# Optimization experiments

Measured on AMD Instinct MI355X. Metric: run time of the kernel, lower is better.

## Reference

```python
import jax, jax.numpy as jnp
import numpy as np

B, T, IN = 4, 1024, 172
D, H, FF, L, NCLS = 512, 8, 2048, 8, 1296
HD = D // H
EPS = 1e-5


def setup_inputs() -> dict:
    key = jax.random.key(0)
    ks = jax.random.split(key, 16)
    rn = lambda k, s, sc=0.02: jax.random.normal(k, s, jnp.float32) * sc
    return {
        "poses": jax.random.normal(ks[0], (B, T, IN), jnp.float32),
        "pose_w": rn(ks[1], (D, IN)), "pose_b": jnp.zeros((D,), jnp.float32),
        "in_w": rn(ks[2], (L, 3 * D, D)), "in_b": jnp.zeros((L, 3 * D), jnp.float32),
        "out_w": rn(ks[3], (L, D, D)), "out_b": jnp.zeros((L, D), jnp.float32),
        "ln1_g": jnp.ones((L, D), jnp.float32), "ln1_b": jnp.zeros((L, D), jnp.float32),
        "ffn_w1": rn(ks[4], (L, FF, D)), "ffn_b1": jnp.zeros((L, FF), jnp.float32),
        "ffn_w2": rn(ks[5], (L, D, FF)), "ffn_b2": jnp.zeros((L, D), jnp.float32),
        "ln2_g": jnp.ones((L, D), jnp.float32), "ln2_b": jnp.zeros((L, D), jnp.float32),
        "tcn1_w": rn(ks[6], (512, D, 5)), "tcn1_b": jnp.zeros((512,), jnp.float32),
        "tcn2_w": rn(ks[7], (D, 512, 5)), "tcn2_b": jnp.zeros((D,), jnp.float32),
        "fc1_w": rn(ks[8], (128, D)), "fc1_b": jnp.zeros((128,), jnp.float32),
        "fc2_w": rn(ks[9], (NCLS, 128)), "fc2_b": jnp.zeros((NCLS,), jnp.float32),
    }


def _pos_enc(seq_len, d):
    # PositionalEncoding1D: interleaved sin/cos per frequency pair
    inv_freq = 1.0 / (10000.0 ** (jnp.arange(0, d, 2, dtype=jnp.float32) / d))
    ang = jnp.arange(seq_len, dtype=jnp.float32)[:, None] * inv_freq  # [T, d/2]
    return jnp.stack([jnp.sin(ang), jnp.cos(ang)], axis=-1).reshape(seq_len, d)


def _ln(x, g, b):
    m = x.mean(-1, keepdims=True)
    v = jnp.var(x, axis=-1, keepdims=True)
    return (x - m) * jax.lax.rsqrt(v + EPS) * g + b


def _encoder_layer(x, iw, ib, ow, ob, g1, b1, w1, c1, w2, c2, g2, b2):
    # post-norm TransformerEncoderLayer, eager (non-flash) attention
    Bc, Tc, _ = x.shape
    qkv = x @ iw.T + ib                       # [B,T,3D]
    q, k, v = jnp.split(qkv, 3, axis=-1)
    q = q.reshape(Bc, Tc, H, HD)
    k = k.reshape(Bc, Tc, H, HD)
    v = v.reshape(Bc, Tc, H, HD)
    scores = jnp.einsum('bqhd,bkhd->bhqk', q, k) / jnp.sqrt(jnp.float32(HD))
    attn = jax.nn.softmax(scores, axis=-1)    # explicit weights (need_weights=True)
    o = jnp.einsum('bhqk,bkhd->bqhd', attn, v).reshape(Bc, Tc, D)
    o = o @ ow.T + ob
    x = _ln(x + o, g1, b1)
    f = jax.nn.relu(x @ w1.T + c1) @ w2.T + c2
    return _ln(x + f, g2, b2)


def _conv1d(x, w, b):  # x [B,T,C_in], w [C_out,C_in,5], pad=2
    y = jax.lax.conv_general_dilated(
        x.transpose(0, 2, 1), w, window_strides=(1,), padding=((2, 2),),
        dimension_numbers=('NCH', 'OIH', 'NCH'))
    return y.transpose(0, 2, 1) + b


def _avgpool2(x):  # kernel=2 stride=2 along time
    Bc, Tc, C = x.shape
    return x.reshape(Bc, Tc // 2, 2, C).mean(axis=2)


def reference(poses, pose_w, pose_b, in_w, in_b, out_w, out_b, ln1_g, ln1_b,
              ffn_w1, ffn_b1, ffn_w2, ffn_b2, ln2_g, ln2_b,
              tcn1_w, tcn1_b, tcn2_w, tcn2_b, fc1_w, fc1_b, fc2_w, fc2_b):
    x = poses.reshape(poses.shape[0], poses.shape[1], -1) @ pose_w.T + pose_b
    x = x + _pos_enc(x.shape[1], D)[None]

    def run_stack(h, idx):
        for i in idx:
            h = _encoder_layer(h, in_w[i], in_b[i], out_w[i], out_b[i],
                               ln1_g[i], ln1_b[i], ffn_w1[i], ffn_b1[i],
                               ffn_w2[i], ffn_b2[i], ln2_g[i], ln2_b[i])
        return h

    h = run_stack(x, (0, 1))
    h = run_stack(h, (2, 3)) + h
    h = run_stack(h, (4, 5)) + h
    h = run_stack(h, (6, 7)) + h

    h = _avgpool2(h)                 # [B,T/2,D]
    h = _conv1d(h, tcn1_w, tcn1_b)   # [B,T/2,512]
    h = _avgpool2(h)                 # [B,T/4,512]
    h = _conv1d(h, tcn2_w, tcn2_b)   # [B,T/4,D]
    h = h @ fc1_w.T + fc1_b
    logits = h @ fc2_w.T + fc2_b     # [B,T/4,num_classes]
    return logits
```

## Files before the change

### kernel.cpp

```cpp
#include <hip/hip_runtime.h>
#include <hip/hip_bf16.h>

static constexpr int kB = 4;
static constexpr int kT = 1024;
static constexpr int kIn = 172;
static constexpr int kD = 512;
static constexpr int kH = 8;
static constexpr int kHD = 64;
static constexpr int kFF = 2048;
static constexpr int kNCLS = 1296;
static constexpr float kEps = 1e-5f;

typedef __attribute__((ext_vector_type(8))) short bf16x8_t;
typedef __attribute__((ext_vector_type(4))) float f32x4_t;
typedef __attribute__((ext_vector_type(8))) unsigned short u16x8_t;
typedef __attribute__((ext_vector_type(4))) unsigned short u16x4_t;

static __device__ __forceinline__ unsigned short f2bf(float f) {
  unsigned int u = __float_as_uint(f);
  unsigned int r = (u + 0x7fffu + ((u >> 16) & 1u)) >> 16;
  return (unsigned short)r;
}

__global__ void cvt_kernel(const float* __restrict__ src, ushort* __restrict__ dst, int n8)
{
  const int i = blockIdx.x * 256 + threadIdx.x;
  if (i >= n8) return;
  const float4 a = *(const float4*)&src[i * 8];
  const float4 b = *(const float4*)&src[i * 8 + 4];
  u16x8_t t;
  t[0] = f2bf(a.x); t[1] = f2bf(a.y); t[2] = f2bf(a.z); t[3] = f2bf(a.w);
  t[4] = f2bf(b.x); t[5] = f2bf(b.y); t[6] = f2bf(b.z); t[7] = f2bf(b.w);
  *(u16x8_t*)&dst[i * 8] = t;
}

template<int MREP, int NREP>
__global__ __launch_bounds__(256) void bgemm_kernel(
    const ushort* __restrict__ A, const ushort* __restrict__ W,
    const float* __restrict__ bias, const float* __restrict__ resid,
    float* __restrict__ C, ushort* __restrict__ Cb, int M, int N, int K, int doRelu)
{
  constexpr int BM = MREP * 32, BN = NREP * 32;
  constexpr int SRD = 72;
  constexpr int TPRA = 256 / BM, CSA = 64 / TPRA, NLA = CSA / 8;
  constexpr int TPRB = 256 / BN, CSB = 64 / TPRB, NLB = CSB / 8;
  __shared__ ushort As[BM * SRD];
  __shared__ ushort Bs[BN * SRD];

  const int tid = threadIdx.x;
  int bid = blockIdx.y * gridDim.x + blockIdx.x;
  const int nwg = gridDim.x * gridDim.y;
  if ((nwg & 7) == 0) bid = (bid & 7) * (nwg >> 3) + (bid >> 3);
  const int bm = (bid / gridDim.x) * BM, bn = (bid % gridDim.x) * BN;

  const int wv = tid >> 6, lane = tid & 63;
  const int lr = lane & 15, lg = lane >> 4;
  const int wr = wv >> 1, wc = wv & 1;

  const int ra = tid / TPRA, ca = (tid % TPRA) * CSA;
  const int rb = tid / TPRB, cb = (tid % TPRB) * CSB;

  f32x4_t acc[MREP][NREP];
#pragma unroll
  for (int mr = 0; mr < MREP; ++mr)
#pragma unroll
    for (int nr = 0; nr < NREP; ++nr) acc[mr][nr] = (f32x4_t){0.f, 0.f, 0.f, 0.f};

  u16x8_t pa[NLA], pb[NLB];
  auto loadAB = [&](int k0) {
    const ushort* ap = A + (size_t)(bm + ra) * K + k0 + ca;
#pragma unroll
    for (int j = 0; j < NLA; ++j) pa[j] = *(const u16x8_t*)(ap + j * 8);
    const ushort* bp = W + (size_t)(bn + rb) * K + k0 + cb;
#pragma unroll
    for (int j = 0; j < NLB; ++j) pb[j] = *(const u16x8_t*)(bp + j * 8);
  };
  auto storeLDS = [&]() {
#pragma unroll
    for (int j = 0; j < NLA; ++j) *(u16x8_t*)&As[ra * SRD + ca + j * 8] = pa[j];
#pragma unroll
    for (int j = 0; j < NLB; ++j) *(u16x8_t*)&Bs[rb * SRD + cb + j * 8] = pb[j];
  };

  loadAB(0);
  storeLDS();
  __syncthreads();

  const int nsteps = K >> 6;
  for (int s = 0; s < nsteps; ++s) {
    const bool more = (s + 1) < nsteps;
    if (more) loadAB((s + 1) << 6);

#pragma unroll
    for (int kk = 0; kk < 2; ++kk) {
      bf16x8_t af[MREP];
#pragma unroll
      for (int mr = 0; mr < MREP; ++mr)
        af[mr] = *(const bf16x8_t*)&As[(wr * MREP * 16 + mr * 16 + lr) * SRD + kk * 32 + lg * 8];
#pragma unroll
      for (int nr = 0; nr < NREP; ++nr) {
        const bf16x8_t bf = *(const bf16x8_t*)&Bs[(wc * NREP * 16 + nr * 16 + lr) * SRD + kk * 32 + lg * 8];
#pragma unroll
        for (int mr = 0; mr < MREP; ++mr)
          acc[mr][nr] = __builtin_amdgcn_mfma_f32_16x16x32_bf16(af[mr], bf, acc[mr][nr], 0, 0, 0);
      }
    }
    __syncthreads();
    if (more) { storeLDS(); __syncthreads(); }
  }

#pragma unroll
  for (int mr = 0; mr < MREP; ++mr) {
#pragma unroll
    for (int v = 0; v < 4; ++v) {
      const int m = bm + wr * MREP * 16 + mr * 16 + lg * 4 + v;
#pragma unroll
      for (int nr = 0; nr < NREP; ++nr) {
        const int n = bn + wc * NREP * 16 + nr * 16 + lr;
        float val = acc[mr][nr][v] + bias[n];
        if (doRelu) val = fmaxf(val, 0.f);
        if (resid) val += resid[(size_t)m * N + n];
        if (C)  C[(size_t)m * N + n] = val;
        if (Cb) Cb[(size_t)m * N + n] = f2bf(val);
      }
    }
  }
}

#define GBM 64
#define GBN 64
#define GBK 16
#define LDST 68

__global__ __launch_bounds__(256) void gemm_kernel(
    const float* __restrict__ A, const float* __restrict__ W,
    const float* __restrict__ bias, const float* __restrict__ resid,
    float* __restrict__ C, int M, int N, int K, int doRelu)
{
  __shared__ __align__(16) float As[GBK][LDST];
  __shared__ __align__(16) float Ws[GBK][LDST];
  const int tid = threadIdx.x;
  const int bm = blockIdx.y * GBM;
  const int bn = blockIdx.x * GBN;
  const int tx = tid & 15, ty = tid >> 4;
  const int li = tid >> 2;
  const int lk = (tid & 3) << 2;

  float acc[4][4];
#pragma unroll
  for (int i = 0; i < 4; ++i)
#pragma unroll
    for (int j = 0; j < 4; ++j) acc[i][j] = 0.f;

  for (int k0 = 0; k0 < K; k0 += GBK) {
    float4 av = make_float4(0.f, 0.f, 0.f, 0.f);
    float4 wv = make_float4(0.f, 0.f, 0.f, 0.f);
    {
      const int m = bm + li;
      if (m < M) {
        if (k0 + lk + 4 <= K) {
          av = *(const float4*)&A[(size_t)m * K + k0 + lk];
        } else {
          float t4[4] = {0.f, 0.f, 0.f, 0.f};
          for (int c = 0; c < 4; ++c) { int k = k0 + lk + c; if (k < K) t4[c] = A[(size_t)m * K + k]; }
          av = make_float4(t4[0], t4[1], t4[2], t4[3]);
        }
      }
      const int n = bn + li;
      if (n < N) {
        if (k0 + lk + 4 <= K) {
          wv = *(const float4*)&W[(size_t)n * K + k0 + lk];
        } else {
          float t4[4] = {0.f, 0.f, 0.f, 0.f};
          for (int c = 0; c < 4; ++c) { int k = k0 + lk + c; if (k < K) t4[c] = W[(size_t)n * K + k]; }
          wv = make_float4(t4[0], t4[1], t4[2], t4[3]);
        }
      }
    }
    __syncthreads();
    As[lk + 0][li] = av.x; As[lk + 1][li] = av.y; As[lk + 2][li] = av.z; As[lk + 3][li] = av.w;
    Ws[lk + 0][li] = wv.x; Ws[lk + 1][li] = wv.y; Ws[lk + 2][li] = wv.z; Ws[lk + 3][li] = wv.w;
    __syncthreads();
#pragma unroll
    for (int kk = 0; kk < GBK; ++kk) {
      const float4 a4 = *(const float4*)&As[kk][ty << 2];
      const float4 b4 = *(const float4*)&Ws[kk][tx << 2];
      const float a[4] = {a4.x, a4.y, a4.z, a4.w};
      const float b[4] = {b4.x, b4.y, b4.z, b4.w};
#pragma unroll
      for (int i = 0; i < 4; ++i)
#pragma unroll
        for (int j = 0; j < 4; ++j) acc[i][j] = fmaf(a[i], b[j], acc[i][j]);
    }
  }

#pragma unroll
  for (int i = 0; i < 4; ++i) {
    const int m = bm + (ty << 2) + i;
    if (m >= M) continue;
#pragma unroll
    for (int j = 0; j < 4; ++j) {
      const int n = bn + (tx << 2) + j;
      if (n >= N) continue;
      float v = acc[i][j] + bias[n];
      if (doRelu) v = fmaxf(v, 0.f);
      if (resid) v += resid[(size_t)m * N + n];
      C[(size_t)m * N + n] = v;
    }
  }
}

__global__ __launch_bounds__(256) void ln_kernel(
    float* __restrict__ X, ushort* __restrict__ Xb,
    const float* __restrict__ g, const float* __restrict__ bta,
    const float* Padd, float* Pout)
{
  const int row = blockIdx.x;
  const int tid = threadIdx.x;
  float* xr = X + (size_t)row * kD;
  const float x0 = xr[tid];
  const float x1 = xr[tid + 256];
  float s = x0 + x1;
  float q = x0 * x0 + x1 * x1;
#pragma unroll
  for (int off = 32; off > 0; off >>= 1) {
    s += __shfl_down(s, off);
    q += __shfl_down(q, off);
  }
  __shared__ float ss[4], qq[4];
  const int w = tid >> 6;
  if ((tid & 63) == 0) { ss[w] = s; qq[w] = q; }
  __syncthreads();
  const float S = ss[0] + ss[1] + ss[2] + ss[3];
  const float Q = qq[0] + qq[1] + qq[2] + qq[3];
  const float mean = S * (1.f / kD);
  const float var = Q * (1.f / kD) - mean * mean;
  const float inv = rsqrtf(var + kEps);
  float v0 = (x0 - mean) * inv * g[tid] + bta[tid];
  float v1 = (x1 - mean) * inv * g[tid + 256] + bta[tid + 256];
  if (Padd) {
    v0 += Padd[(size_t)row * kD + tid];
    v1 += Padd[(size_t)row * kD + tid + 256];
  }
  xr[tid] = v0; xr[tid + 256] = v1;
  ushort* xb = Xb + (size_t)row * kD;
  xb[tid] = f2bf(v0); xb[tid + 256] = f2bf(v1);
  if (Pout) {
    Pout[(size_t)row * kD + tid] = v0;
    Pout[(size_t)row * kD + tid + 256] = v1;
  }
}

#define KSTR 72
#define PSTR 74
__global__ __launch_bounds__(256) void attn_mfma_kernel(
    const ushort* __restrict__ qkv, ushort* __restrict__ O)
{
  const int b = blockIdx.z, h = blockIdx.y;
  const int q0 = blockIdx.x << 6;
  const int tid = threadIdx.x;
  const int wv = tid >> 6, lane = tid & 63;
  const int lr = lane & 15;
  const int lg = lane >> 4;

  __shared__ ushort Ks[64 * KSTR];
  __shared__ ushort Vt[64 * KSTR];
  __shared__ ushort Pl[4][16 * PSTR];

  bf16x8_t qa[2];
  {
    const ushort* qrow = qkv + ((size_t)(b * kT + q0 + wv * 16 + lr)) * (3 * kD) + h * kHD + lg * 8;
    qa[0] = *(const bf16x8_t*)qrow;
    qa[1] = *(const bf16x8_t*)(qrow + 32);
  }

  float m_[4], l_[4];
  f32x4_t oacc[4];
#pragma unroll
  for (int r = 0; r < 4; ++r) { m_[r] = -1e30f; l_[r] = 0.f; }
#pragma unroll
  for (int nb = 0; nb < 4; ++nb) oacc[nb] = (f32x4_t){0.f, 0.f, 0.f, 0.f};

  const int srow = tid >> 2;
  const int sd   = (tid & 3) << 4;
  const int vkp  = tid & 31;
  const int vdh  = tid >> 5;

  for (int kt = 0; kt < kT / 64; ++kt) {
    __syncthreads();
    {
      const ushort* kr = qkv + ((size_t)(b * kT + (kt << 6) + srow)) * (3 * kD) + kD + h * kHD + sd;
      *(u16x8_t*)&Ks[srow * KSTR + sd]     = *(const u16x8_t*)kr;
      *(u16x8_t*)&Ks[srow * KSTR + sd + 8] = *(const u16x8_t*)(kr + 8);
      const ushort* vr = qkv + ((size_t)(b * kT + (kt << 6) + 2 * vkp)) * (3 * kD) + 2 * kD + h * kHD + vdh * 8;
      const u16x8_t v0 = *(const u16x8_t*)vr;
      const u16x8_t v1 = *(const u16x8_t*)(vr + 3 * kD);
#pragma unroll
      for (int e = 0; e < 8; ++e) {
        const unsigned int packv = (unsigned int)v0[e] | ((unsigned int)v1[e] << 16);
        *(unsigned int*)&Vt[(vdh * 8 + e) * KSTR + 2 * vkp] = packv;
      }
    }
    __syncthreads();

    f32x4_t s[4];
#pragma unroll
    for (int cc = 0; cc < 4; ++cc) {
      const ushort* kb = &Ks[(cc * 16 + lr) * KSTR + lg * 8];
      const bf16x8_t k0 = *(const bf16x8_t*)kb;
      const bf16x8_t k1 = *(const bf16x8_t*)(kb + 32);
      f32x4_t acc = (f32x4_t){0.f, 0.f, 0.f, 0.f};
      acc = __builtin_amdgcn_mfma_f32_16x16x32_bf16(qa[0], k0, acc, 0, 0, 0);
      acc = __builtin_amdgcn_mfma_f32_16x16x32_bf16(qa[1], k1, acc, 0, 0, 0);
#pragma unroll
      for (int r = 0; r < 4; ++r) acc[r] *= 0.125f;
      s[cc] = acc;
    }

#pragma unroll
    for (int r = 0; r < 4; ++r) {
      float mx = fmaxf(fmaxf(s[0][r], s[1][r]), fmaxf(s[2][r], s[3][r]));
      mx = fmaxf(mx, __shfl_xor(mx, 1));
      mx = fmaxf(mx, __shfl_xor(mx, 2));
      mx = fmaxf(mx, __shfl_xor(mx, 4));
      mx = fmaxf(mx, __shfl_xor(mx, 8));
      const float mnew = fmaxf(m_[r], mx);
      const float alpha = __expf(m_[r] - mnew);
      float sum = 0.f;
#pragma unroll
      for (int cc = 0; cc < 4; ++cc) {
        const float p = __expf(s[cc][r] - mnew);
        s[cc][r] = p;
        sum += p;
      }
      sum += __shfl_xor(sum, 1);
      sum += __shfl_xor(sum, 2);
      sum += __shfl_xor(sum, 4);
      sum += __shfl_xor(sum, 8);
      l_[r] = l_[r] * alpha + sum;
      m_[r] = mnew;
#pragma unroll
      for (int nb = 0; nb < 4; ++nb) oacc[nb][r] *= alpha;
#pragma unroll
      for (int cc = 0; cc < 4; ++cc)
        Pl[wv][(lg * 4 + r) * PSTR + cc * 16 + lr] = f2bf(s[cc][r]);
    }

    const bf16x8_t pa0 = *(const bf16x8_t*)&Pl[wv][lr * PSTR + lg * 8];
    const bf16x8_t pa1 = *(const bf16x8_t*)&Pl[wv][lr * PSTR + 32 + lg * 8];
#pragma unroll
    for (int nb = 0; nb < 4; ++nb) {
      const ushort* vb = &Vt[(nb * 16 + lr) * KSTR + lg * 8];
      const bf16x8_t v0 = *(const bf16x8_t*)vb;
      const bf16x8_t v1 = *(const bf16x8_t*)(vb + 32);
      oacc[nb] = __builtin_amdgcn_mfma_f32_16x16x32_bf16(pa0, v0, oacc[nb], 0, 0, 0);
      oacc[nb] = __builtin_amdgcn_mfma_f32_16x16x32_bf16(pa1, v1, oacc[nb], 0, 0, 0);
    }
  }

#pragma unroll
  for (int nb = 0; nb < 4; ++nb) {
#pragma unroll
    for (int r = 0; r < 4; ++r) {
      const int row = lg * 4 + r;
      const int col = nb * 16 + lr;
      O[((size_t)(b * kT + q0 + wv * 16 + row)) * kD + h * kHD + col] = f2bf(oacc[nb][r] / l_[r]);
    }
  }
}

__global__ __launch_bounds__(256) void posenc_kernel(float* __restrict__ X, ushort* __restrict__ Xb)
{
  const int bt = blockIdx.x;
  const int t = bt & (kT - 1);
  float* row = X + (size_t)bt * kD;
  ushort* rb = Xb + (size_t)bt * kD;
#pragma unroll
  for (int p = 0; p < 2; ++p) {
    const int d = threadIdx.x + p * 256;
    const int j = d >> 1;
    const float inv = expf(-(float)j * 0.03597789207803197f);
    const float ang = (float)t * inv;
    const float pe = (d & 1) ? cosf(ang) : sinf(ang);
    const float v = row[d] + pe;
    row[d] = v;
    rb[d] = f2bf(v);
  }
}

__global__ void im2col_pool_kernel(const float* __restrict__ X, ushort* __restrict__ X5,
                                   int Tt, int n4)
{
  const int idx = blockIdx.x * 256 + threadIdx.x;
  if (idx >= n4) return;
  const int ci4 = idx & 127;
  int r = idx >> 7;
  const int tap = r % 5; r /= 5;
  const int t = r % Tt;
  const int b = r / Tt;
  const int ts = t + tap - 2;
  u16x4_t o = (u16x4_t){0, 0, 0, 0};
  if (ts >= 0 && ts < Tt) {
    const float* p = X + ((size_t)(b * 2 * Tt + 2 * ts)) * kD + ci4 * 4;
    const float4 x0 = *(const float4*)p;
    const float4 x1 = *(const float4*)(p + kD);
    o[0] = f2bf(0.5f * (x0.x + x1.x)); o[1] = f2bf(0.5f * (x0.y + x1.y));
    o[2] = f2bf(0.5f * (x0.z + x1.z)); o[3] = f2bf(0.5f * (x0.w + x1.w));
  }
  *(u16x4_t*)&X5[((size_t)(b * Tt + t)) * 2560 + tap * kD + ci4 * 4] = o;
}

__global__ void convw_t_kernel(const float* __restrict__ w, ushort* __restrict__ Wt)
{
  const int idx = blockIdx.x * 256 + threadIdx.x;
  if (idx >= 512 * 512 * 5) return;
  const int ci = idx & 511;
  int r = idx >> 9;
  const int tap = r % 5;
  const int co = r / 5;
  Wt[(size_t)co * 2560 + tap * 512 + ci] = f2bf(w[(size_t)co * 2560 + ci * 5 + tap]);
}

extern "C" void kernel_launch(void* const* d_in, const int* in_sizes, int n_in,
                              void* d_out, int out_size, void* d_ws, size_t ws_size,
                              hipStream_t stream)
{
  (void)in_sizes; (void)n_in; (void)out_size;
  const float* poses  = (const float*)d_in[0];
  const float* pose_w = (const float*)d_in[1];
  const float* pose_b = (const float*)d_in[2];
  const float* in_w   = (const float*)d_in[3];
  const float* in_b   = (const float*)d_in[4];
  const float* out_w  = (const float*)d_in[5];
  const float* out_b  = (const float*)d_in[6];
  const float* ln1_g  = (const float*)d_in[7];
  const float* ln1_b  = (const float*)d_in[8];
  const float* ffn_w1 = (const float*)d_in[9];
  const float* ffn_b1 = (const float*)d_in[10];
  const float* ffn_w2 = (const float*)d_in[11];
  const float* ffn_b2 = (const float*)d_in[12];
  const float* ln2_g  = (const float*)d_in[13];
  const float* ln2_b  = (const float*)d_in[14];
  const float* tcn1_w = (const float*)d_in[15];
  const float* tcn1_b = (const float*)d_in[16];
  const float* tcn2_w = (const float*)d_in[17];
  const float* tcn2_b = (const float*)d_in[18];
  const float* fc1_w  = (const float*)d_in[19];
  const float* fc1_b  = (const float*)d_in[20];
  const float* fc2_w  = (const float*)d_in[21];
  const float* fc2_b  = (const float*)d_in[22];

  char* base = (char*)d_ws;
  float*  A    = (float*)(base);
  float*  Y    = (float*)(base + 8388608);
  float*  P    = (float*)(base + 16777216);
  ushort* Abf  = (ushort*)(base + 25165824);
  ushort* QKV  = (ushort*)(base + 29360128);
  ushort* Ybf  = QKV;
  ushort* X5   = QKV;
  ushort* MID  = (ushort*)(base + 41943040);
  ushort* ATTb = MID;
  ushort* CW   = MID;
  ushort* Wbf  = (ushort*)(base + 58720256);

  const size_t nWq = (size_t)3 * kD * kD;
  const size_t nWo = (size_t)kD * kD;
  const size_t nW1 = (size_t)kFF * kD;
  const size_t nW2 = (size_t)kD * kFF;
  const size_t nWl = nWq + nWo + nW1 + nW2;
  const bool fullW = ws_size >= (size_t)58720256 + nWl * 8 * 2;

  const int M = kB * kT;
  dim3 blk(256);
  auto cvt = [&](const float* s, ushort* d, size_t n) {
    cvt_kernel<<<(int)((n / 8 + 255) / 256), blk, 0, stream>>>(s, d, (int)(n / 8));
  };

  if (fullW) {
    cvt(in_w,   Wbf,                        nWq * 8);
    cvt(out_w,  Wbf + nWq * 8,              nWo * 8);
    cvt(ffn_w1, Wbf + nWq * 8 + nWo * 8,    nW1 * 8);
    cvt(ffn_w2, Wbf + (nWq + nWo + nW1) * 8, nW2 * 8);
  }

  gemm_kernel<<<dim3(kD / GBN, M / GBM), blk, 0, stream>>>(poses, pose_w, pose_b, nullptr, A, M, kD, kIn, 0);
  posenc_kernel<<<M, blk, 0, stream>>>(A, Abf);

  for (int l = 0; l < 8; ++l) {
    const ushort *Wq, *Wo, *W1, *W2;
    if (fullW) {
      Wq = Wbf + (size_t)l * nWq;
      Wo = Wbf + nWq * 8 + (size_t)l * nWo;
      W1 = Wbf + nWq * 8 + nWo * 8 + (size_t)l * nW1;
      W2 = Wbf + (nWq + nWo + nW1) * 8 + (size_t)l * nW2;
    } else {
      cvt(in_w   + (size_t)l * nWq, Wbf, nWq);
      cvt(out_w  + (size_t)l * nWo, Wbf + nWq, nWo);
      cvt(ffn_w1 + (size_t)l * nW1, Wbf + nWq + nWo, nW1);
      cvt(ffn_w2 + (size_t)l * nW2, Wbf + nWq + nWo + nW1, nW2);
      Wq = Wbf; Wo = Wbf + nWq; W1 = Wbf + nWq + nWo; W2 = Wbf + nWq + nWo + nW1;
    }

    bgemm_kernel<4, 4><<<dim3(3 * kD / 128, M / 128), blk, 0, stream>>>(
        Abf, Wq, in_b + (size_t)l * 3 * kD, nullptr, nullptr, QKV, M, 3 * kD, kD, 0);
    attn_mfma_kernel<<<dim3(kT / 64, kH, kB), blk, 0, stream>>>(QKV, ATTb);
    bgemm_kernel<2, 4><<<dim3(kD / 128, M / 64), blk, 0, stream>>>(
        ATTb, Wo, out_b + (size_t)l * kD, A, Y, nullptr, M, kD, kD, 0);
    ln_kernel<<<M, blk, 0, stream>>>(Y, Ybf, ln1_g + (size_t)l * kD, ln1_b + (size_t)l * kD,
                                     nullptr, nullptr);
    bgemm_kernel<4, 4><<<dim3(kFF / 128, M / 128), blk, 0, stream>>>(
        Ybf, W1, ffn_b1 + (size_t)l * kFF, nullptr, nullptr, MID, M, kFF, kD, 1);
    bgemm_kernel<2, 4><<<dim3(kD / 128, M / 64), blk, 0, stream>>>(
        MID, W2, ffn_b2 + (size_t)l * kD, Y, A, nullptr, M, kD, kFF, 0);
    {
      const float* padd = (l == 3 || l == 5 || l == 7) ? P : nullptr;
      float* pout = (l == 1 || l == 3 || l == 5) ? P : nullptr;
      ln_kernel<<<M, blk, 0, stream>>>(A, Abf, ln2_g + (size_t)l * kD, ln2_b + (size_t)l * kD,
                                       padd, pout);
    }
  }

  {
    const int T1 = kT / 2;
    const int T2 = kT / 4;
    convw_t_kernel<<<(512 * 512 * 5 + 255) / 256, blk, 0, stream>>>(tcn1_w, CW);
    const int n4a = kB * T1 * 5 * (kD / 4);
    im2col_pool_kernel<<<(n4a + 255) / 256, blk, 0, stream>>>(A, X5, T1, n4a);
    bgemm_kernel<2, 2><<<dim3(kD / 64, kB * T1 / 64), blk, 0, stream>>>(
        X5, CW, tcn1_b, nullptr, Y, nullptr, kB * T1, kD, 2560, 0);
    convw_t_kernel<<<(512 * 512 * 5 + 255) / 256, blk, 0, stream>>>(tcn2_w, CW);
    const int n4b = kB * T2 * 5 * (kD / 4);
    im2col_pool_kernel<<<(n4b + 255) / 256, blk, 0, stream>>>(Y, X5, T2, n4b);
    bgemm_kernel<2, 2><<<dim3(kD / 64, kB * T2 / 64), blk, 0, stream>>>(
        X5, CW, tcn2_b, nullptr, A, nullptr, kB * T2, kD, 2560, 0);
    const int Mh = kB * T2;
    gemm_kernel<<<dim3(128 / GBN, Mh / GBM), blk, 0, stream>>>(A, fc1_w, fc1_b, nullptr, Y, Mh, 128, kD, 0);
    gemm_kernel<<<dim3((kNCLS + GBN - 1) / GBN, Mh / GBM), blk, 0, stream>>>(
        Y, fc2_w, fc2_b, nullptr, (float*)d_out, Mh, kNCLS, 128, 0);
  }
}
```

Baseline: 1.458 ms.

## Use direct global-to-LDS loads in bf16 GEMM and prefetch K/V in attention

The bf16 GEMM now stages A and W tiles with global_load_lds (direct global-to-shared DMA) and a K-step of 32, in an unpadded LDS layout, instead of register-staged loads into padded 64-wide tiles. The attention kernel prefetches the next K/V tile into registers while computing on the current one. Several GEMM launches move to 4x2 tile shapes. The unpadded LDS layout may cause bank conflicts, and the single-buffered global_load_lds with a smaller K step adds more barriers per unit of work.

```diff
diff --git a/kernel.cpp b/kernel.cpp
--- a/kernel.cpp
+++ b/kernel.cpp
@@ -34,18 +34,17 @@
   *(u16x8_t*)&dst[i * 8] = t;
 }
 
-template<int MREP, int NREP>
+template<int MR, int NR>
 __global__ __launch_bounds__(256) void bgemm_kernel(
     const ushort* __restrict__ A, const ushort* __restrict__ W,
     const float* __restrict__ bias, const float* __restrict__ resid,
     float* __restrict__ C, ushort* __restrict__ Cb, int M, int N, int K, int doRelu)
 {
-  constexpr int BM = MREP * 32, BN = NREP * 32;
-  constexpr int SRD = 72;
-  constexpr int TPRA = 256 / BM, CSA = 64 / TPRA, NLA = CSA / 8;
-  constexpr int TPRB = 256 / BN, CSB = 64 / TPRB, NLB = CSB / 8;
-  __shared__ ushort As[BM * SRD];
-  __shared__ ushort Bs[BN * SRD];
+  constexpr int BM = MR * 32, BN = NR * 32, BK = 32;
+  constexpr int AI = BM / 64;
+  constexpr int BI = BN / 64;
+  __shared__ ushort As[BM * BK];
+  __shared__ ushort Bs[BN * BK];
 
   const int tid = threadIdx.x;
   int bid = blockIdx.y * gridDim.x + blockIdx.x;
@@ -57,71 +56,67 @@
   const int lr = lane & 15, lg = lane >> 4;
   const int wr = wv >> 1, wc = wv & 1;
 
-  const int ra = tid / TPRA, ca = (tid % TPRA) * CSA;
-  const int rb = tid / TPRB, cb = (tid % TPRB) * CSB;
-
-  f32x4_t acc[MREP][NREP];
-#pragma unroll
-  for (int mr = 0; mr < MREP; ++mr)
-#pragma unroll
-    for (int nr = 0; nr < NREP; ++nr) acc[mr][nr] = (f32x4_t){0.f, 0.f, 0.f, 0.f};
-
-  u16x8_t pa[NLA], pb[NLB];
-  auto loadAB = [&](int k0) {
-    const ushort* ap = A + (size_t)(bm + ra) * K + k0 + ca;
-#pragma unroll
-    for (int j = 0; j < NLA; ++j) pa[j] = *(const u16x8_t*)(ap + j * 8);
-    const ushort* bp = W + (size_t)(bn + rb) * K + k0 + cb;
-#pragma unroll
-    for (int j = 0; j < NLB; ++j) pb[j] = *(const u16x8_t*)(bp + j * 8);
+  const int arow0 = wv * (BM / 4);
+  const int brow0 = wv * (BN / 4);
+  const int lrow = lane >> 2;
+  const int lchunk = (lane & 3) * 8;
+
+  f32x4_t acc[MR][NR];
+#pragma unroll
+  for (int m = 0; m < MR; ++m)
+#pragma unroll
+    for (int n = 0; n < NR; ++n) acc[m][n] = (f32x4_t){0.f, 0.f, 0.f, 0.f};
+
+  auto stage = [&](int k0) {
+#pragma unroll
+    for (int i = 0; i < AI; ++i) {
+      const ushort* g = A + (size_t)(bm + arow0 + i * 16 + lrow) * K + k0 + lchunk;
+      __builtin_amdgcn_global_load_lds(
+          (const __attribute__((address_space(1))) void*)g,
+          (__attribute__((address_space(3))) void*)&As[(arow0 + i * 16) * BK], 16, 0, 0);
+    }
+#pragma unroll
+    for (int i = 0; i < BI; ++i) {
+      const ushort* g = W + (size_t)(bn + brow0 + i * 16 + lrow) * K + k0 + lchunk;
+      __builtin_amdgcn_global_load_lds(
+          (const __attribute__((address_space(1))) void*)g,
+          (__attribute__((address_space(3))) void*)&Bs[(brow0 + i * 16) * BK], 16, 0, 0);
+    }
   };
-  auto storeLDS = [&]() {
-#pragma unroll
-    for (int j = 0; j < NLA; ++j) *(u16x8_t*)&As[ra * SRD + ca + j * 8] = pa[j];
-#pragma unroll
-    for (int j = 0; j < NLB; ++j) *(u16x8_t*)&Bs[rb * SRD + cb + j * 8] = pb[j];
-  };
-
-  loadAB(0);
-  storeLDS();
-  __syncthreads();
-
-  const int nsteps = K >> 6;
+
+  stage(0);
+  const int nsteps = K >> 5;
   for (int s = 0; s < nsteps; ++s) {
-    const bool more = (s + 1) < nsteps;
-    if (more) loadAB((s + 1) << 6);
-
-#pragma unroll
-    for (int kk = 0; kk < 2; ++kk) {
-      bf16x8_t af[MREP];
-#pragma unroll
-      for (int mr = 0; mr < MREP; ++mr)
-        af[mr] = *(const bf16x8_t*)&As[(wr * MREP * 16 + mr * 16 + lr) * SRD + kk * 32 + lg * 8];
-#pragma unroll
-      for (int nr = 0; nr < NREP; ++nr) {
-        const bf16x8_t bf = *(const bf16x8_t*)&Bs[(wc * NREP * 16 + nr * 16 + lr) * SRD + kk * 32 + lg * 8];
-#pragma unroll
-        for (int mr = 0; mr < MREP; ++mr)
-          acc[mr][nr] = __builtin_amdgcn_mfma_f32_16x16x32_bf16(af[mr], bf, acc[mr][nr], 0, 0, 0);
-      }
-    }
     __syncthreads();
-    if (more) { storeLDS(); __syncthreads(); }
-  }
-
-#pragma unroll
-  for (int mr = 0; mr < MREP; ++mr) {
+    bf16x8_t af[MR], bf[NR];
+#pragma unroll
+    for (int m = 0; m < MR; ++m)
+      af[m] = *(const bf16x8_t*)&As[(wr * MR * 16 + m * 16 + lr) * BK + lg * 8];
+#pragma unroll
+    for (int n = 0; n < NR; ++n)
+      bf[n] = *(const bf16x8_t*)&Bs[(wc * NR * 16 + n * 16 + lr) * BK + lg * 8];
+#pragma unroll
+    for (int n = 0; n < NR; ++n)
+#pragma unroll
+      for (int m = 0; m < MR; ++m)
+        acc[m][n] = __builtin_amdgcn_mfma_f32_16x16x32_bf16(af[m], bf[n], acc[m][n], 0, 0, 0);
+    __syncthreads();
+    if (s + 1 < nsteps) stage((s + 1) << 5);
+  }
+
+#pragma unroll
+  for (int m = 0; m < MR; ++m) {
 #pragma unroll
     for (int v = 0; v < 4; ++v) {
-      const int m = bm + wr * MREP * 16 + mr * 16 + lg * 4 + v;
-#pragma unroll
-      for (int nr = 0; nr < NREP; ++nr) {
-        const int n = bn + wc * NREP * 16 + nr * 16 + lr;
-        float val = acc[mr][nr][v] + bias[n];
+      const int mm = bm + wr * MR * 16 + m * 16 + lg * 4 + v;
+#pragma unroll
+      for (int n = 0; n < NR; ++n) {
+        const int nn = bn + wc * NR * 16 + n * 16 + lr;
+        float val = acc[m][n][v] + bias[nn];
         if (doRelu) val = fmaxf(val, 0.f);
-        if (resid) val += resid[(size_t)m * N + n];
-        if (C)  C[(size_t)m * N + n] = val;
-        if (Cb) Cb[(size_t)m * N + n] = f2bf(val);
+        if (resid) val += resid[(size_t)mm * N + nn];
+        if (C)  C[(size_t)mm * N + nn] = val;
+        if (Cb) Cb[(size_t)mm * N + nn] = f2bf(val);
       }
     }
   }
@@ -286,32 +281,40 @@
   const int vkp  = tid & 31;
   const int vdh  = tid >> 5;
 
+  u16x8_t k0_, k1_, v0_, v1_;
+  auto load_regs = [&](int kt) {
+    const ushort* kr = qkv + ((size_t)(b * kT + (kt << 6) + srow)) * (3 * kD) + kD + h * kHD + sd;
+    k0_ = *(const u16x8_t*)kr;
+    k1_ = *(const u16x8_t*)(kr + 8);
+    const ushort* vr = qkv + ((size_t)(b * kT + (kt << 6) + 2 * vkp)) * (3 * kD) + 2 * kD + h * kHD + vdh * 8;
+    v0_ = *(const u16x8_t*)vr;
+    v1_ = *(const u16x8_t*)(vr + 3 * kD);
+  };
+
+  load_regs(0);
   for (int kt = 0; kt < kT / 64; ++kt) {
     __syncthreads();
     {
-      const ushort* kr = qkv + ((size_t)(b * kT + (kt << 6) + srow)) * (3 * kD) + kD + h * kHD + sd;
-      *(u16x8_t*)&Ks[srow * KSTR + sd]     = *(const u16x8_t*)kr;
-      *(u16x8_t*)&Ks[srow * KSTR + sd + 8] = *(const u16x8_t*)(kr + 8);
-      const ushort* vr = qkv + ((size_t)(b * kT + (kt << 6) + 2 * vkp)) * (3 * kD) + 2 * kD + h * kHD + vdh * 8;
-      const u16x8_t v0 = *(const u16x8_t*)vr;
-      const u16x8_t v1 = *(const u16x8_t*)(vr + 3 * kD);
+      *(u16x8_t*)&Ks[srow * KSTR + sd]     = k0_;
+      *(u16x8_t*)&Ks[srow * KSTR + sd + 8] = k1_;
 #pragma unroll
       for (int e = 0; e < 8; ++e) {
-        const unsigned int packv = (unsigned int)v0[e] | ((unsigned int)v1[e] << 16);
+        const unsigned int packv = (unsigned int)v0_[e] | ((unsigned int)v1_[e] << 16);
         *(unsigned int*)&Vt[(vdh * 8 + e) * KSTR + 2 * vkp] = packv;
       }
     }
     __syncthreads();
+    if (kt + 1 < kT / 64) load_regs(kt + 1);
 
     f32x4_t s[4];
 #pragma unroll
     for (int cc = 0; cc < 4; ++cc) {
       const ushort* kb = &Ks[(cc * 16 + lr) * KSTR + lg * 8];
-      const bf16x8_t k0 = *(const bf16x8_t*)kb;
-      const bf16x8_t k1 = *(const bf16x8_t*)(kb + 32);
+      const bf16x8_t kf0 = *(const bf16x8_t*)kb;
+      const bf16x8_t kf1 = *(const bf16x8_t*)(kb + 32);
       f32x4_t acc = (f32x4_t){0.f, 0.f, 0.f, 0.f};
-      acc = __builtin_amdgcn_mfma_f32_16x16x32_bf16(qa[0], k0, acc, 0, 0, 0);
-      acc = __builtin_amdgcn_mfma_f32_16x16x32_bf16(qa[1], k1, acc, 0, 0, 0);
+      acc = __builtin_amdgcn_mfma_f32_16x16x32_bf16(qa[0], kf0, acc, 0, 0, 0);
+      acc = __builtin_amdgcn_mfma_f32_16x16x32_bf16(qa[1], kf1, acc, 0, 0, 0);
 #pragma unroll
       for (int r = 0; r < 4; ++r) acc[r] *= 0.125f;
       s[cc] = acc;
@@ -351,10 +354,10 @@
 #pragma unroll
     for (int nb = 0; nb < 4; ++nb) {
       const ushort* vb = &Vt[(nb * 16 + lr) * KSTR + lg * 8];
-      const bf16x8_t v0 = *(const bf16x8_t*)vb;
-      const bf16x8_t v1 = *(const bf16x8_t*)(vb + 32);
-      oacc[nb] = __builtin_amdgcn_mfma_f32_16x16x32_bf16(pa0, v0, oacc[nb], 0, 0, 0);
-      oacc[nb] = __builtin_amdgcn_mfma_f32_16x16x32_bf16(pa1, v1, oacc[nb], 0, 0, 0);
+      const bf16x8_t vf0 = *(const bf16x8_t*)vb;
+      const bf16x8_t vf1 = *(const bf16x8_t*)(vb + 32);
+      oacc[nb] = __builtin_amdgcn_mfma_f32_16x16x32_bf16(pa0, vf0, oacc[nb], 0, 0, 0);
+      oacc[nb] = __builtin_amdgcn_mfma_f32_16x16x32_bf16(pa1, vf1, oacc[nb], 0, 0, 0);
     }
   }
 
@@ -504,13 +507,13 @@
     bgemm_kernel<4, 4><<<dim3(3 * kD / 128, M / 128), blk, 0, stream>>>(
         Abf, Wq, in_b + (size_t)l * 3 * kD, nullptr, nullptr, QKV, M, 3 * kD, kD, 0);
     attn_mfma_kernel<<<dim3(kT / 64, kH, kB), blk, 0, stream>>>(QKV, ATTb);
-    bgemm_kernel<2, 4><<<dim3(kD / 128, M / 64), blk, 0, stream>>>(
+    bgemm_kernel<4, 2><<<dim3(kD / 64, M / 128), blk, 0, stream>>>(
         ATTb, Wo, out_b + (size_t)l * kD, A, Y, nullptr, M, kD, kD, 0);
     ln_kernel<<<M, blk, 0, stream>>>(Y, Ybf, ln1_g + (size_t)l * kD, ln1_b + (size_t)l * kD,
                                      nullptr, nullptr);
     bgemm_kernel<4, 4><<<dim3(kFF / 128, M / 128), blk, 0, stream>>>(
         Ybf, W1, ffn_b1 + (size_t)l * kFF, nullptr, nullptr, MID, M, kFF, kD, 1);
-    bgemm_kernel<2, 4><<<dim3(kD / 128, M / 64), blk, 0, stream>>>(
+    bgemm_kernel<4, 2><<<dim3(kD / 64, M / 128), blk, 0, stream>>>(
         MID, W2, ffn_b2 + (size_t)l * kD, Y, A, nullptr, M, kD, kFF, 0);
     {
       const float* padd = (l == 3 || l == 5 || l == 7) ? P : nullptr;
@@ -526,12 +529,12 @@
     convw_t_kernel<<<(512 * 512 * 5 + 255) / 256, blk, 0, stream>>>(tcn1_w, CW);
     const int n4a = kB * T1 * 5 * (kD / 4);
     im2col_pool_kernel<<<(n4a + 255) / 256, blk, 0, stream>>>(A, X5, T1, n4a);
-    bgemm_kernel<2, 2><<<dim3(kD / 64, kB * T1 / 64), blk, 0, stream>>>(
+    bgemm_kernel<4, 2><<<dim3(kD / 64, kB * T1 / 128), blk, 0, stream>>>(
         X5, CW, tcn1_b, nullptr, Y, nullptr, kB * T1, kD, 2560, 0);
     convw_t_kernel<<<(512 * 512 * 5 + 255) / 256, blk, 0, stream>>>(tcn2_w, CW);
     const int n4b = kB * T2 * 5 * (kD / 4);
     im2col_pool_kernel<<<(n4b + 255) / 256, blk, 0, stream>>>(Y, X5, T2, n4b);
-    bgemm_kernel<2, 2><<<dim3(kD / 64, kB * T2 / 64), blk, 0, stream>>>(
+    bgemm_kernel<4, 2><<<dim3(kD / 64, kB * T2 / 128), blk, 0, stream>>>(
         X5, CW, tcn2_b, nullptr, A, nullptr, kB * T2, kD, 2560, 0);
     const int Mh = kB * T2;
     gemm_kernel<<<dim3(128 / GBN, Mh / GBM), blk, 0, stream>>>(A, fc1_w, fc1_b, nullptr, Y, Mh, 128, kD, 0);
```

Measured after the change: 1.561 ms. 7.1% more time.
